# Kernel tuning notes

Measured on AMD Instinct MI355X. Metric: run time of the kernel, lower is better.

The kernel has to match this reference:

```python
import jax, jax.numpy as jnp
import numpy as np

N, E, Q = 50000, 800000, 2000000   # nodes, edges, quadruplets
F_IN, H, OUT, G = 128, 128, 1, 64  # in_channels, hidden, out_channels, graphs
NRBF = NCBF = NSBF = 6
L = 3  # num_layers


def _mlp2(h, Wa, ba, Wb, bb):
    # Linear -> ReLU -> Linear
    return jax.nn.relu(h @ Wa + ba) @ Wb + bb


def setup_inputs() -> dict:
    key = jax.random.key(0)
    ks = jax.random.split(key, 24)
    s = 0.05
    inp = {
        "x": jax.random.normal(ks[0], (N, F_IN), jnp.float32),
        "rbf": jax.random.normal(ks[1], (E, NRBF), jnp.float32),
        "cbf": jax.random.normal(ks[2], (Q, NCBF), jnp.float32),
        "sbf": jax.random.normal(ks[3], (Q, NSBF), jnp.float32),
        "edge_index": jax.random.randint(ks[4], (2, E), 0, N),
        "l_idx": jax.random.randint(ks[5], (Q,), 0, N),
        "k_idx": jax.random.randint(ks[6], (Q,), 0, E),
        "batch": jnp.sort(jax.random.randint(ks[7], (N,), 0, G)),
        # per-layer params (all layers share shapes since F_IN == H)
        "W_e1a": s * jax.random.normal(ks[8], (L, F_IN + NRBF + NCBF + NSBF, H)),
        "b_e1a": jnp.zeros((L, H)),
        "W_e1b": s * jax.random.normal(ks[9], (L, H, H)),
        "b_e1b": jnp.zeros((L, H)),
        "W_e2a": s * jax.random.normal(ks[10], (L, 2 * H, H)),
        "b_e2a": jnp.zeros((L, H)),
        "W_e2b": s * jax.random.normal(ks[11], (L, H, H)),
        "b_e2b": jnp.zeros((L, H)),
        "W_na": s * jax.random.normal(ks[12], (L, F_IN + H, H)),
        "b_na": jnp.zeros((L, H)),
        "W_nb": s * jax.random.normal(ks[13], (L, H, H)),
        "b_nb": jnp.zeros((L, H)),
        "W_oa": s * jax.random.normal(ks[14], (H, H)),
        "b_oa": jnp.zeros((H,)),
        "W_ob": s * jax.random.normal(ks[15], (H, OUT)),
        "b_ob": jnp.zeros((OUT,)),
    }
    return inp


def reference(x, rbf, cbf, sbf,
              W_e1a, b_e1a, W_e1b, b_e1b,
              W_e2a, b_e2a, W_e2b, b_e2b,
              W_na, b_na, W_nb, b_nb,
              W_oa, b_oa, W_ob, b_ob,
              edge_index, l_idx, k_idx, batch):
    src, dst = edge_index[0], edge_index[1]  # x_j = x[src], index = dst
    h = x
    for p in range(L):
        # quadruplet message: gather-concat-MLP  [Q, F+18] -> [Q, H]
        m_in = jnp.concatenate([h[l_idx], rbf[k_idx], cbf, sbf], axis=-1)
        em = _mlp2(m_in, W_e1a[p], b_e1a[p], W_e1b[p], b_e1b[p])
        # scatter-add quadruplet messages onto edges by k_idx -> [E, H]
        agg_e = jax.ops.segment_sum(em, k_idx, num_segments=E)
        # second stage: per-edge concat (note: aggregated indexed by dst, as in source)
        fin = jnp.concatenate([h[src], agg_e[dst]], axis=-1)
        msg = _mlp2(fin, W_e2a[p], b_e2a[p], W_e2b[p], b_e2b[p])
        # aggregate edge messages to target nodes -> [N, H]
        aggr = jax.ops.segment_sum(msg, dst, num_segments=N)
        h = _mlp2(jnp.concatenate([h, aggr], axis=-1), W_na[p], b_na[p], W_nb[p], b_nb[p])
    # global mean pool over graphs
    counts = jax.ops.segment_sum(jnp.ones((N, 1), h.dtype), batch, num_segments=G)
    pooled = jax.ops.segment_sum(h, batch, num_segments=G) / jnp.maximum(counts, 1.0)
    pooled = jax.nn.relu(pooled)
    return _mlp2(pooled, W_oa, b_oa, W_ob, b_ob)
```

## Files before the change

kernel.cpp:

```cpp
#include <hip/hip_runtime.h>

constexpr int Nn = 50000;
constexpr int Ee = 800000;
constexpr int Qq = 2000000;
constexpr int Gg = 64;
constexpr int Hh = 128;
constexpr int NB64 = (Nn + 63) / 64;
constexpr int NSCB = (Nn + 1023) / 1024;

typedef short bf16x8 __attribute__((ext_vector_type(8)));
typedef float f32x4  __attribute__((ext_vector_type(4)));

__device__ __forceinline__ unsigned short f2bf(float f) {
    unsigned u = __builtin_bit_cast(unsigned, f);
    u += 0x7FFFu + ((u >> 16) & 1u);
    return (unsigned short)(u >> 16);
}
__device__ __forceinline__ float bf2f(unsigned short s) {
    unsigned u = ((unsigned)s) << 16;
    return __builtin_bit_cast(float, u);
}

__global__ void k_hist(const int* __restrict__ idx, int n, int limit,
                       int* __restrict__ hist) {
    int i = blockIdx.x * blockDim.x + threadIdx.x;
    if (i < n) { int v = idx[i]; if (v < limit) atomicAdd(&hist[v], 1); }
}

__global__ __launch_bounds__(1024) void k_scanA(const int* __restrict__ hist,
                                                int* __restrict__ cursor,
                                                int* __restrict__ bsum) {
    __shared__ int s[1024];
    const int tid = threadIdx.x;
    int i = blockIdx.x * 1024 + tid;
    int v = (i < Nn) ? hist[i] : 0;
    s[tid] = v;
    __syncthreads();
    for (int off = 1; off < 1024; off <<= 1) {
        int t = (tid >= off) ? s[tid - off] : 0;
        __syncthreads();
        s[tid] += t;
        __syncthreads();
    }
    if (i < Nn) cursor[i] = s[tid] - v;
    if (tid == 1023) bsum[blockIdx.x] = s[1023];
}
__global__ void k_scanB(int* __restrict__ bsum) {
    __shared__ int s[64];
    const int tid = threadIdx.x;
    int v = (tid < NSCB) ? bsum[tid] : 0;
    s[tid] = v;
    __syncthreads();
    for (int off = 1; off < 64; off <<= 1) {
        int t = (tid >= off) ? s[tid - off] : 0;
        __syncthreads();
        s[tid] += t;
        __syncthreads();
    }
    if (tid < NSCB) bsum[tid] = s[tid] - v;
}
__global__ __launch_bounds__(1024) void k_scanC(int* __restrict__ cursor,
                                                const int* __restrict__ bsum) {
    int i = blockIdx.x * 1024 + threadIdx.x;
    if (i < Nn) cursor[i] += bsum[blockIdx.x];
}

__global__ void k_scatter_e(const int* __restrict__ dst, const int* __restrict__ src,
                            int* __restrict__ cursor, int* __restrict__ srcs) {
    int i = blockIdx.x * blockDim.x + threadIdx.x;
    if (i < Ee) {
        int v = dst[i];
        int p = atomicAdd(&cursor[v], 1);
        srcs[p] = src[i];
    }
}

__global__ void k_scatter_q(const int* __restrict__ k_idx, const int* __restrict__ l_idx,
                            const float* __restrict__ cbf, const float* __restrict__ sbf,
                            int* __restrict__ cursor,
                            int* __restrict__ lq, unsigned short* __restrict__ qfeat) {
    int i = blockIdx.x * blockDim.x + threadIdx.x;
    if (i >= Qq) return;
    int v = k_idx[i];
    if (v >= Nn) return;
    int p = atomicAdd(&cursor[v], 1);
    lq[p] = l_idx[i];
    unsigned short f[12];
#pragma unroll
    for (int k = 0; k < 6; ++k) f[k] = f2bf(cbf[(size_t)i * 6 + k]);
#pragma unroll
    for (int k = 0; k < 6; ++k) f[6 + k] = f2bf(sbf[(size_t)i * 6 + k]);
    *(uint2*)&qfeat[(size_t)p * 12]     = *(uint2*)&f[0];
    *(uint2*)&qfeat[(size_t)p * 12 + 4] = *(uint2*)&f[4];
    *(uint2*)&qfeat[(size_t)p * 12 + 8] = *(uint2*)&f[8];
}

__global__ void k_wtall(const float* __restrict__ We1a0, const float* __restrict__ We1b0,
                        const float* __restrict__ We2a0, const float* __restrict__ We2b0,
                        const float* __restrict__ Wna0,  const float* __restrict__ Wnb0,
                        unsigned short* __restrict__ wbuf) {
    int idx = blockIdx.x * blockDim.x + threadIdx.x;
    if (idx >= 135168) return;
    const int p = blockIdx.y;
    const float* We1a = We1a0 + (size_t)p * 146 * 128;
    const float* We1b = We1b0 + (size_t)p * 128 * 128;
    const float* We2a = We2a0 + (size_t)p * 256 * 128;
    const float* We2b = We2b0 + (size_t)p * 128 * 128;
    const float* Wna  = Wna0  + (size_t)p * 256 * 128;
    const float* Wnb  = Wnb0  + (size_t)p * 128 * 128;
    unsigned short* base = wbuf + (size_t)p * 135168;
    const float* src; int K, Kp, loc;
    if (idx < 16384)       { src = We1a;             K = 128; Kp = 128; loc = idx; }
    else if (idx < 20480)  { src = We1a + 128 * 128; K = 6;   Kp = 32;  loc = idx - 16384; }
    else if (idx < 36864)  { src = We1b;             K = 128; Kp = 128; loc = idx - 20480; }
    else if (idx < 69632)  { src = We2a;             K = 256; Kp = 256; loc = idx - 36864; }
    else if (idx < 86016)  { src = We2b;             K = 128; Kp = 128; loc = idx - 69632; }
    else if (idx < 118784) { src = Wna;              K = 256; Kp = 256; loc = idx - 86016; }
    else                   { src = Wnb;              K = 128; Kp = 128; loc = idx - 118784; }
    int n = loc / Kp, k = loc - n * Kp;
    base[idx] = (k < K) ? f2bf(src[(size_t)k * 128 + n]) : (unsigned short)0;
}

__global__ void k_h0(const float* __restrict__ x, unsigned short* __restrict__ hb) {
    int idx = blockIdx.x * blockDim.x + threadIdx.x;
    if (idx < Nn * Hh) hb[idx] = f2bf(x[idx]);
}

__device__ __forceinline__ void zacc(f32x4 acc[4][2]) {
#pragma unroll
    for (int rt = 0; rt < 4; ++rt)
#pragma unroll
        for (int ct = 0; ct < 2; ++ct)
            acc[rt][ct] = (f32x4){0.f, 0.f, 0.f, 0.f};
}

template<int KK, int SA, int KP>
__device__ __forceinline__ void gemm64(const unsigned short* A,
                                       const unsigned short* __restrict__ Wt,
                                       int k_off, f32x4 acc[4][2]) {
    const int tid = threadIdx.x;
    const int lane = tid & 63;
    const int nb = (tid >> 6) * 32;
    const int rA = lane & 15;
    const int kg = lane >> 4;
#pragma unroll
    for (int ks = 0; ks < KK / 32; ++ks) {
        const int ka = ks * 32 + kg * 8;
        const int kb = k_off + ka;
        bf16x8 b0 = *(const bf16x8*)&Wt[(size_t)(nb + rA) * KP + kb];
        bf16x8 b1 = *(const bf16x8*)&Wt[(size_t)(nb + 16 + rA) * KP + kb];
#pragma unroll
        for (int rt = 0; rt < 4; ++rt) {
            bf16x8 a = *(const bf16x8*)&A[(rt * 16 + rA) * SA + ka];
            acc[rt][0] = __builtin_amdgcn_mfma_f32_16x16x32_bf16(a, b0, acc[rt][0], 0, 0, 0);
            acc[rt][1] = __builtin_amdgcn_mfma_f32_16x16x32_bf16(a, b1, acc[rt][1], 0, 0, 0);
        }
    }
}

__device__ __forceinline__ void store_acc(const f32x4 acc[4][2], unsigned short* out,
                                          int n0, int nmax) {
    const int tid = threadIdx.x;
    const int lane = tid & 63;
    const int nb = (tid >> 6) * 32;
    const int rA = lane & 15, kg = lane >> 4;
#pragma unroll
    for (int rt = 0; rt < 4; ++rt)
#pragma unroll
        for (int ct = 0; ct < 2; ++ct) {
            int col = nb + ct * 16 + rA;
#pragma unroll
            for (int i = 0; i < 4; ++i) {
                int n = n0 + rt * 16 + kg * 4 + i;
                if (n < nmax) out[(size_t)n * 128 + col] = f2bf(acc[rt][ct][i]);
            }
        }
}

__global__ __launch_bounds__(256) void k_pre(
    const unsigned short* __restrict__ hb, const float* __restrict__ rbf,
    const unsigned short* __restrict__ wb,
    unsigned short* __restrict__ P1, unsigned short* __restrict__ Z1,
    unsigned short* __restrict__ P2)
{
    __shared__ unsigned short L[64 * 136];
    const int m0 = blockIdx.x * 64;
    const int tid = threadIdx.x;
    const unsigned short* Wq1t = wb;
    const unsigned short* Wp2t = wb + 16384;
    const unsigned short* We2at = wb + 36864;
    for (int i = tid; i < 64 * 16; i += 256) {
        int row = i >> 4, ch = i & 15;
        int n = min(m0 + row, Nn - 1);
        *(uint4*)&L[row * 136 + ch * 8] = *(const uint4*)&hb[(size_t)n * 128 + ch * 8];
    }
    __syncthreads();
    f32x4 acc[4][2];
    zacc(acc);
    gemm64<128, 136, 128>(L, Wq1t, 0, acc);
    store_acc(acc, P1, m0, Nn);
    zacc(acc);
    gemm64<128, 136, 256>(L, We2at, 0, acc);
    store_acc(acc, Z1, m0, Nn);
    __syncthreads();
    for (int i = tid; i < 64 * 32; i += 256) {
        int row = i >> 5, c = i & 31;
        int n = min(m0 + row, Nn - 1);
        float v = (c < 6) ? rbf[(size_t)n * 6 + c] : 0.f;
        L[row * 136 + c] = f2bf(v);
    }
    __syncthreads();
    zacc(acc);
    gemm64<32, 136, 32>(L, Wp2t, 0, acc);
    store_acc(acc, P2, m0, Nn);
}

__global__ __launch_bounds__(256) void k_quadagg(
    const unsigned short* __restrict__ P1, const unsigned short* __restrict__ P2,
    const unsigned short* __restrict__ qfeat, const int* __restrict__ lq,
    const int* __restrict__ rowend, const int* __restrict__ rowcnt,
    const float* __restrict__ We1a_raw, const float* __restrict__ b_e1a,
    unsigned short* __restrict__ Rb)
{
    __shared__ float W34[12 * 128];
    __shared__ float bia[128];
    const int tid = threadIdx.x;
    for (int i = tid; i < 12 * 128; i += 256) W34[i] = We1a_raw[134 * 128 + i];
    if (tid < 128) bia[tid] = b_e1a[tid];
    __syncthreads();
    const int nd = tid >> 4;
    const int c0 = (tid & 15) * 8;
    const int n = blockIdx.x * 16 + nd;
    const int end = rowend[n];
    const int beg = end - rowcnt[n];
    float base[8];
    {
        uint4 p2v = *(const uint4*)&P2[(size_t)n * 128 + c0];
        const unsigned short* pp = (const unsigned short*)&p2v;
#pragma unroll
        for (int k = 0; k < 8; ++k) base[k] = bia[c0 + k] + bf2f(pp[k]);
    }
    float acc[8];
#pragma unroll
    for (int k = 0; k < 8; ++k) acc[k] = 0.f;
    for (int e = beg; e < end; ++e) {
        int l = lq[e];
        uint4 a = *(const uint4*)&P1[(size_t)l * 128 + c0];
        uint2 f0 = *(const uint2*)&qfeat[(size_t)e * 12];
        uint2 f1 = *(const uint2*)&qfeat[(size_t)e * 12 + 4];
        uint2 f2 = *(const uint2*)&qfeat[(size_t)e * 12 + 8];
        const unsigned short* q0 = (const unsigned short*)&f0;
        const unsigned short* q1 = (const unsigned short*)&f1;
        const unsigned short* q2 = (const unsigned short*)&f2;
        float qv[12] = {bf2f(q0[0]), bf2f(q0[1]), bf2f(q0[2]), bf2f(q0[3]),
                        bf2f(q1[0]), bf2f(q1[1]), bf2f(q1[2]), bf2f(q1[3]),
                        bf2f(q2[0]), bf2f(q2[1]), bf2f(q2[2]), bf2f(q2[3])};
        const unsigned short* ap = (const unsigned short*)&a;
        float t[8];
#pragma unroll
        for (int k = 0; k < 8; ++k) t[k] = base[k] + bf2f(ap[k]);
#pragma unroll
        for (int kk = 0; kk < 12; ++kk) {
            float q_ = qv[kk];
#pragma unroll
            for (int k = 0; k < 8; ++k)
                t[k] = fmaf(q_, W34[kk * 128 + c0 + k], t[k]);
        }
#pragma unroll
        for (int k = 0; k < 8; ++k) acc[k] += fmaxf(t[k], 0.f);
    }
    unsigned short ov[8];
#pragma unroll
    for (int k = 0; k < 8; ++k) ov[k] = f2bf(acc[k]);
    *(uint4*)&Rb[(size_t)n * 128 + c0] = *(uint4*)ov;
}

__global__ __launch_bounds__(256) void k_edgeagg(
    const unsigned short* __restrict__ Z1, const unsigned short* __restrict__ Z2,
    const int* __restrict__ srcs,
    const int* __restrict__ rowend, const int* __restrict__ rowcnt,
    const float* __restrict__ b_e2a,
    unsigned short* __restrict__ Rb)
{
    const int tid = threadIdx.x;
    const int nd = tid >> 4;
    const int c0 = (tid & 15) * 8;
    const int n = blockIdx.x * 16 + nd;
    const int end = rowend[n];
    const int beg = end - rowcnt[n];
    float z2b[8];
    {
        uint4 zv = *(const uint4*)&Z2[(size_t)n * 128 + c0];
        const unsigned short* zp = (const unsigned short*)&zv;
        float4 b0 = *(const float4*)&b_e2a[c0];
        float4 b1 = *(const float4*)&b_e2a[c0 + 4];
        z2b[0] = b0.x + bf2f(zp[0]); z2b[1] = b0.y + bf2f(zp[1]);
        z2b[2] = b0.z + bf2f(zp[2]); z2b[3] = b0.w + bf2f(zp[3]);
        z2b[4] = b1.x + bf2f(zp[4]); z2b[5] = b1.y + bf2f(zp[5]);
        z2b[6] = b1.z + bf2f(zp[6]); z2b[7] = b1.w + bf2f(zp[7]);
    }
    float acc[8];
#pragma unroll
    for (int k = 0; k < 8; ++k) acc[k] = 0.f;
    int e = beg;
    for (; e + 2 <= end; e += 2) {
        int s0 = srcs[e], s1 = srcs[e + 1];
        uint4 a0 = *(const uint4*)&Z1[(size_t)s0 * 128 + c0];
        uint4 a1 = *(const uint4*)&Z1[(size_t)s1 * 128 + c0];
        const unsigned short* p0 = (const unsigned short*)&a0;
        const unsigned short* p1 = (const unsigned short*)&a1;
#pragma unroll
        for (int k = 0; k < 8; ++k) acc[k] += fmaxf(z2b[k] + bf2f(p0[k]), 0.f);
#pragma unroll
        for (int k = 0; k < 8; ++k) acc[k] += fmaxf(z2b[k] + bf2f(p1[k]), 0.f);
    }
    if (e < end) {
        int s0 = srcs[e];
        uint4 a0 = *(const uint4*)&Z1[(size_t)s0 * 128 + c0];
        const unsigned short* p0 = (const unsigned short*)&a0;
#pragma unroll
        for (int k = 0; k < 8; ++k) acc[k] += fmaxf(z2b[k] + bf2f(p0[k]), 0.f);
    }
    unsigned short ov[8];
#pragma unroll
    for (int k = 0; k < 8; ++k) ov[k] = f2bf(acc[k]);
    *(uint4*)&Rb[(size_t)n * 128 + c0] = *(uint4*)ov;
}

__global__ __launch_bounds__(256) void k_agg2z(
    const unsigned short* __restrict__ Rb, const int* __restrict__ cntq,
    const unsigned short* __restrict__ wb, const float* __restrict__ b_e1b,
    unsigned short* __restrict__ Z2)
{
    __shared__ unsigned short L[64 * 136];
    __shared__ int rc[64];
    const int m0 = blockIdx.x * 64;
    const int tid = threadIdx.x;
    const unsigned short* We1bt = wb + 20480;
    const unsigned short* We2at = wb + 36864;
    if (tid < 64) rc[tid] = (m0 + tid < Nn) ? cntq[m0 + tid] : 0;
    for (int i = tid; i < 64 * 16; i += 256) {
        int row = i >> 4, ch = i & 15;
        int n = min(m0 + row, Nn - 1);
        *(uint4*)&L[row * 136 + ch * 8] = *(const uint4*)&Rb[(size_t)n * 128 + ch * 8];
    }
    __syncthreads();
    f32x4 acc[4][2];
    zacc(acc);
    gemm64<128, 136, 128>(L, We1bt, 0, acc);
    __syncthreads();
    {
        const int lane = tid & 63;
        const int nb = (tid >> 6) * 32;
        const int rA = lane & 15, kg = lane >> 4;
#pragma unroll
        for (int rt = 0; rt < 4; ++rt)
#pragma unroll
            for (int ct = 0; ct < 2; ++ct) {
                int col = nb + ct * 16 + rA;
                float bias = b_e1b[col];
#pragma unroll
                for (int i = 0; i < 4; ++i) {
                    int row = rt * 16 + kg * 4 + i;
                    L[row * 136 + col] = f2bf(acc[rt][ct][i] + (float)rc[row] * bias);
                }
            }
    }
    __syncthreads();
    zacc(acc);
    gemm64<128, 136, 256>(L, We2at, 128, acc);
    store_acc(acc, Z2, m0, Nn);
}

__global__ __launch_bounds__(256) void k_nodeNew(
    const unsigned short* __restrict__ Rb, const int* __restrict__ deg,
    const unsigned short* __restrict__ wb,
    const float* __restrict__ b_e2b, const float* __restrict__ b_na,
    const float* __restrict__ b_nb,
    unsigned short* __restrict__ hb)
{
    __shared__ unsigned short L[64 * 136];
    __shared__ int rc[64];
    const int m0 = blockIdx.x * 64;
    const int tid = threadIdx.x;
    const unsigned short* We2bt = wb + 69632;
    const unsigned short* Wnat  = wb + 86016;
    const unsigned short* Wnbt  = wb + 118784;
    const int lane = tid & 63;
    const int nb = (tid >> 6) * 32;
    const int rA = lane & 15, kg = lane >> 4;
    if (tid < 64) rc[tid] = (m0 + tid < Nn) ? deg[m0 + tid] : 0;
    for (int i = tid; i < 64 * 16; i += 256) {
        int row = i >> 4, ch = i & 15;
        int n = min(m0 + row, Nn - 1);
        *(uint4*)&L[row * 136 + ch * 8] = *(const uint4*)&Rb[(size_t)n * 128 + ch * 8];
    }
    __syncthreads();
    f32x4 acc[4][2];
    zacc(acc);
    gemm64<128, 136, 128>(L, We2bt, 0, acc);
    __syncthreads();
#pragma unroll
    for (int rt = 0; rt < 4; ++rt)
#pragma unroll
        for (int ct = 0; ct < 2; ++ct) {
            int col = nb + ct * 16 + rA;
            float bias = b_e2b[col];
#pragma unroll
            for (int i = 0; i < 4; ++i) {
                int row = rt * 16 + kg * 4 + i;
                L[row * 136 + col] = f2bf(acc[rt][ct][i] + (float)rc[row] * bias);
            }
        }
    __syncthreads();
    f32x4 acc2[4][2];
    zacc(acc2);
    gemm64<128, 136, 256>(L, Wnat, 128, acc2);
    __syncthreads();
    for (int i = tid; i < 64 * 16; i += 256) {
        int row = i >> 4, ch = i & 15;
        int n = min(m0 + row, Nn - 1);
        *(uint4*)&L[row * 136 + ch * 8] = *(const uint4*)&hb[(size_t)n * 128 + ch * 8];
    }
    __syncthreads();
    gemm64<128, 136, 256>(L, Wnat, 0, acc2);
    __syncthreads();
#pragma unroll
    for (int rt = 0; rt < 4; ++rt)
#pragma unroll
        for (int ct = 0; ct < 2; ++ct) {
            int col = nb + ct * 16 + rA;
            float bias = b_na[col];
#pragma unroll
            for (int i = 0; i < 4; ++i) {
                int row = rt * 16 + kg * 4 + i;
                L[row * 136 + col] = f2bf(fmaxf(acc2[rt][ct][i] + bias, 0.f));
            }
        }
    __syncthreads();
    zacc(acc);
    gemm64<128, 136, 128>(L, Wnbt, 0, acc);
#pragma unroll
    for (int rt = 0; rt < 4; ++rt)
#pragma unroll
        for (int ct = 0; ct < 2; ++ct) {
            int col = nb + ct * 16 + rA;
            float bias = b_nb[col];
#pragma unroll
            for (int i = 0; i < 4; ++i) {
                int n = m0 + rt * 16 + kg * 4 + i;
                if (n < Nn)
                    hb[(size_t)n * 128 + col] = f2bf(acc[rt][ct][i] + bias);
            }
        }
}

__global__ __launch_bounds__(256) void k_pool(const unsigned short* __restrict__ hb,
                                              const int* __restrict__ batch,
                                              float* __restrict__ pooled,
                                              float* __restrict__ cntg) {
    __shared__ int bseg[200];
    constexpr int CH = 196;
    const int start = blockIdx.x * CH;
    const int end = min(start + CH, Nn);
    if (start >= end) return;
    const int tid = threadIdx.x;
    for (int i = tid; i < end - start; i += 256) bseg[i] = batch[start + i];
    __syncthreads();
    const int j = tid & 127;
    const int rh = tid >> 7;
    float acc = 0.f, cacc = 0.f;
    int cur = -1;
    for (int n = start + rh; n < end; n += 2) {
        int g = bseg[n - start];
        if (g != cur) {
            if (cur >= 0) {
                atomicAdd(&pooled[cur * Hh + j], acc);
                if (j == 0) atomicAdd(&cntg[cur], cacc);
            }
            cur = g; acc = 0.f; cacc = 0.f;
        }
        acc += bf2f(hb[(size_t)n * Hh + j]);
        cacc += 1.f;
    }
    if (cur >= 0) {
        atomicAdd(&pooled[cur * Hh + j], acc);
        if (j == 0) atomicAdd(&cntg[cur], cacc);
    }
}

__global__ __launch_bounds__(128) void k_final(
    const float* __restrict__ pooled, const float* __restrict__ cntg,
    const float* __restrict__ Woa, const float* __restrict__ boa,
    const float* __restrict__ Wob, const float* __restrict__ bob,
    float* __restrict__ out)
{
    __shared__ float p[128];
    __shared__ float t[128];
    __shared__ float red[128];
    const int g = blockIdx.x;
    const int j = threadIdx.x;
    float c = fmaxf(cntg[g], 1.f);
    p[j] = fmaxf(pooled[g * Hh + j] / c, 0.f);
    __syncthreads();
    float acc = boa[j];
    for (int d = 0; d < Hh; ++d) acc = fmaf(p[d], Woa[d * Hh + j], acc);
    t[j] = fmaxf(acc, 0.f);
    __syncthreads();
    red[j] = t[j] * Wob[j];
    __syncthreads();
    for (int s = 64; s > 0; s >>= 1) {
        if (j < s) red[j] += red[j + s];
        __syncthreads();
    }
    if (j == 0) out[g] = red[0] + bob[0];
}

extern "C" void kernel_launch(void* const* d_in, const int* in_sizes, int n_in,
                              void* d_out, int out_size, void* d_ws, size_t ws_size,
                              hipStream_t stream) {
    const float* x     = (const float*)d_in[0];
    const float* rbf   = (const float*)d_in[1];
    const float* cbf   = (const float*)d_in[2];
    const float* sbf   = (const float*)d_in[3];
    const int*   eidx  = (const int*)d_in[4];
    const int*   l_idx = (const int*)d_in[5];
    const int*   k_idx = (const int*)d_in[6];
    const int*   batch = (const int*)d_in[7];
    const float* W_e1a = (const float*)d_in[8];
    const float* b_e1a = (const float*)d_in[9];
    const float* W_e1b = (const float*)d_in[10];
    const float* b_e1b = (const float*)d_in[11];
    const float* W_e2a = (const float*)d_in[12];
    const float* b_e2a = (const float*)d_in[13];
    const float* W_e2b = (const float*)d_in[14];
    const float* b_e2b = (const float*)d_in[15];
    const float* W_na  = (const float*)d_in[16];
    const float* b_na  = (const float*)d_in[17];
    const float* W_nb  = (const float*)d_in[18];
    const float* b_nb  = (const float*)d_in[19];
    const float* W_oa  = (const float*)d_in[20];
    const float* b_oa  = (const float*)d_in[21];
    const float* W_ob  = (const float*)d_in[22];
    const float* b_ob  = (const float*)d_in[23];

    const int* src = eidx;
    const int* dst = eidx + Ee;

    const size_t NHb = (size_t)Nn * Hh * sizeof(unsigned short);
    char* w = (char*)d_ws;
    unsigned short* hb  = (unsigned short*)w; w += NHb;
    unsigned short* P1  = (unsigned short*)w; w += NHb;
    unsigned short* P2  = (unsigned short*)w; w += NHb;
    unsigned short* Z1  = (unsigned short*)w; w += NHb;
    unsigned short* Z2  = (unsigned short*)w; w += NHb;
    unsigned short* Rb  = (unsigned short*)w; w += NHb;
    float* pooled = (float*)w; w += (size_t)Gg * Hh * sizeof(float);
    float* cntg   = (float*)w; w += (size_t)Gg * sizeof(float);
    int*   lq     = (int*)w;   w += (size_t)Qq * sizeof(int);
    unsigned short* qfeat = (unsigned short*)w; w += (size_t)Qq * 12 * sizeof(unsigned short);
    int*   srcs_e = (int*)w;   w += (size_t)Ee * sizeof(int);
    int*   hist_e = (int*)w;   w += (size_t)Nn * sizeof(int);
    int*   hist_q = (int*)w;   w += (size_t)Nn * sizeof(int);
    int*   cur_e  = (int*)w;   w += (size_t)Nn * sizeof(int);
    int*   cur_q  = (int*)w;   w += (size_t)Nn * sizeof(int);
    int*   bsum_e = (int*)w;   w += 64 * sizeof(int);
    int*   bsum_q = (int*)w;   w += 64 * sizeof(int);
    unsigned short* wbuf = (unsigned short*)w;

    const size_t LSTRIDE = 135168;

    hipMemsetAsync(hist_e, 0, Nn * sizeof(int), stream);
    k_hist<<<(Ee + 255) / 256, 256, 0, stream>>>(dst, Ee, Nn, hist_e);
    k_scanA<<<NSCB, 1024, 0, stream>>>(hist_e, cur_e, bsum_e);
    k_scanB<<<1, 64, 0, stream>>>(bsum_e);
    k_scanC<<<NSCB, 1024, 0, stream>>>(cur_e, bsum_e);
    k_scatter_e<<<(Ee + 255) / 256, 256, 0, stream>>>(dst, src, cur_e, srcs_e);
    hipMemsetAsync(hist_q, 0, Nn * sizeof(int), stream);
    k_hist<<<(Qq + 255) / 256, 256, 0, stream>>>(k_idx, Qq, Nn, hist_q);
    k_scanA<<<NSCB, 1024, 0, stream>>>(hist_q, cur_q, bsum_q);
    k_scanB<<<1, 64, 0, stream>>>(bsum_q);
    k_scanC<<<NSCB, 1024, 0, stream>>>(cur_q, bsum_q);
    k_scatter_q<<<(Qq + 255) / 256, 256, 0, stream>>>(k_idx, l_idx, cbf, sbf,
        cur_q, lq, qfeat);

    k_h0<<<(Nn * Hh + 255) / 256, 256, 0, stream>>>(x, hb);

    {
        dim3 g((135168 + 255) / 256, 3);
        k_wtall<<<g, 256, 0, stream>>>(W_e1a, W_e1b, W_e2a, W_e2b, W_na, W_nb, wbuf);
    }

    for (int p = 0; p < 3; ++p) {
        const unsigned short* wb = wbuf + p * LSTRIDE;
        k_pre<<<NB64, 256, 0, stream>>>(hb, rbf, wb, P1, Z1, P2);
        k_quadagg<<<Nn / 16, 256, 0, stream>>>(P1, P2, qfeat, lq,
            cur_q, hist_q, W_e1a + (size_t)p * 146 * 128, b_e1a + (size_t)p * 128, Rb);
        k_agg2z<<<NB64, 256, 0, stream>>>(Rb, hist_q, wb, b_e1b + (size_t)p * 128, Z2);
        k_edgeagg<<<Nn / 16, 256, 0, stream>>>(Z1, Z2, srcs_e, cur_e, hist_e,
            b_e2a + (size_t)p * 128, Rb);
        k_nodeNew<<<NB64, 256, 0, stream>>>(Rb, hist_e, wb,
            b_e2b + (size_t)p * 128, b_na + (size_t)p * 128, b_nb + (size_t)p * 128,
            hb);
    }
    hipMemsetAsync(pooled, 0, (size_t)Gg * Hh * sizeof(float), stream);
    hipMemsetAsync(cntg, 0, (size_t)Gg * sizeof(float), stream);
    k_pool<<<(Nn + 195) / 196, 256, 0, stream>>>(hb, batch, pooled, cntg);
    k_final<<<Gg, 128, 0, stream>>>(pooled, cntg, W_oa, b_oa, W_ob, b_ob, (float*)d_out);
}
```

Before: 572.2 us.

## Fuse per-layer kernels into one megakernel and merge CSR build passes

Merges the per-layer pipeline (quad aggregation, agg2 GEMM, edge aggregation, node update, plus the next layer's P1/Z1 precompute) into a single 64-node-tile kernel that keeps intermediates in shared memory instead of round-tripping Rb/Z2 through global memory. P1/Z1 are double-buffered across layers, and the rbf projection P2 is precomputed for all three layers in an initial kernel that also converts x to bf16. The edge and quad histogram, scan and scatter passes are merged into combined launches to cut launch count. The cost is lower occupancy from the larger shared footprint and register pressure, with only about 782 blocks per layer. Irregular gather work and GEMM work are now serialized inside one block rather than running as separate, well-balanced kernels.

```diff
diff --git a/kernel.cpp b/kernel.cpp
--- a/kernel.cpp
+++ b/kernel.cpp
@@ -21,19 +21,24 @@
     return __builtin_bit_cast(float, u);
 }
 
-__global__ void k_hist(const int* __restrict__ idx, int n, int limit,
-                       int* __restrict__ hist) {
+__global__ void k_hist2(const int* __restrict__ dst, const int* __restrict__ kidx,
+                        int* __restrict__ hist_e, int* __restrict__ hist_q) {
     int i = blockIdx.x * blockDim.x + threadIdx.x;
-    if (i < n) { int v = idx[i]; if (v < limit) atomicAdd(&hist[v], 1); }
-}
-
-__global__ __launch_bounds__(1024) void k_scanA(const int* __restrict__ hist,
-                                                int* __restrict__ cursor,
-                                                int* __restrict__ bsum) {
+    if (i < Ee) atomicAdd(&hist_e[dst[i]], 1);
+    if (i < Qq) { int v = kidx[i]; if (v < Nn) atomicAdd(&hist_q[v], 1); }
+}
+
+__global__ __launch_bounds__(1024) void k_scanA2(const int* __restrict__ he,
+                                                 const int* __restrict__ hq,
+                                                 int* __restrict__ ce, int* __restrict__ cq,
+                                                 int* __restrict__ bs) {
     __shared__ int s[1024];
+    const int* h = blockIdx.y ? hq : he;
+    int* c = blockIdx.y ? cq : ce;
+    int* b = bs + blockIdx.y * 64;
     const int tid = threadIdx.x;
     int i = blockIdx.x * 1024 + tid;
-    int v = (i < Nn) ? hist[i] : 0;
+    int v = (i < Nn) ? h[i] : 0;
     s[tid] = v;
     __syncthreads();
     for (int off = 1; off < 1024; off <<= 1) {
@@ -42,13 +47,14 @@
         s[tid] += t;
         __syncthreads();
     }
-    if (i < Nn) cursor[i] = s[tid] - v;
-    if (tid == 1023) bsum[blockIdx.x] = s[1023];
-}
-__global__ void k_scanB(int* __restrict__ bsum) {
+    if (i < Nn) c[i] = s[tid] - v;
+    if (tid == 1023) b[blockIdx.x] = s[1023];
+}
+__global__ void k_scanB2(int* __restrict__ bs) {
     __shared__ int s[64];
+    int* b = bs + blockIdx.x * 64;
     const int tid = threadIdx.x;
-    int v = (tid < NSCB) ? bsum[tid] : 0;
+    int v = (tid < NSCB) ? b[tid] : 0;
     s[tid] = v;
     __syncthreads();
     for (int off = 1; off < 64; off <<= 1) {
@@ -57,42 +63,42 @@
         s[tid] += t;
         __syncthreads();
     }
-    if (tid < NSCB) bsum[tid] = s[tid] - v;
-}
-__global__ __launch_bounds__(1024) void k_scanC(int* __restrict__ cursor,
-                                                const int* __restrict__ bsum) {
+    if (tid < NSCB) b[tid] = s[tid] - v;
+}
+__global__ __launch_bounds__(1024) void k_scanC2(int* __restrict__ ce, int* __restrict__ cq,
+                                                 const int* __restrict__ bs) {
+    int* c = blockIdx.y ? cq : ce;
+    const int* b = bs + blockIdx.y * 64;
     int i = blockIdx.x * 1024 + threadIdx.x;
-    if (i < Nn) cursor[i] += bsum[blockIdx.x];
-}
-
-__global__ void k_scatter_e(const int* __restrict__ dst, const int* __restrict__ src,
-                            int* __restrict__ cursor, int* __restrict__ srcs) {
+    if (i < Nn) c[i] += b[blockIdx.x];
+}
+
+__global__ void k_scatter_both(const int* __restrict__ dst, const int* __restrict__ src,
+                               const int* __restrict__ kidx, const int* __restrict__ lidx,
+                               const float* __restrict__ cbf, const float* __restrict__ sbf,
+                               int* __restrict__ cur_e, int* __restrict__ cur_q,
+                               int* __restrict__ srcs, int* __restrict__ lq,
+                               unsigned short* __restrict__ qfeat) {
     int i = blockIdx.x * blockDim.x + threadIdx.x;
     if (i < Ee) {
-        int v = dst[i];
-        int p = atomicAdd(&cursor[v], 1);
+        int p = atomicAdd(&cur_e[dst[i]], 1);
         srcs[p] = src[i];
     }
-}
-
-__global__ void k_scatter_q(const int* __restrict__ k_idx, const int* __restrict__ l_idx,
-                            const float* __restrict__ cbf, const float* __restrict__ sbf,
-                            int* __restrict__ cursor,
-                            int* __restrict__ lq, unsigned short* __restrict__ qfeat) {
-    int i = blockIdx.x * blockDim.x + threadIdx.x;
-    if (i >= Qq) return;
-    int v = k_idx[i];
-    if (v >= Nn) return;
-    int p = atomicAdd(&cursor[v], 1);
-    lq[p] = l_idx[i];
-    unsigned short f[12];
-#pragma unroll
-    for (int k = 0; k < 6; ++k) f[k] = f2bf(cbf[(size_t)i * 6 + k]);
-#pragma unroll
-    for (int k = 0; k < 6; ++k) f[6 + k] = f2bf(sbf[(size_t)i * 6 + k]);
-    *(uint2*)&qfeat[(size_t)p * 12]     = *(uint2*)&f[0];
-    *(uint2*)&qfeat[(size_t)p * 12 + 4] = *(uint2*)&f[4];
-    *(uint2*)&qfeat[(size_t)p * 12 + 8] = *(uint2*)&f[8];
+    if (i < Qq) {
+        int v = kidx[i];
+        if (v < Nn) {
+            int p = atomicAdd(&cur_q[v], 1);
+            lq[p] = lidx[i];
+            unsigned short f[12];
+#pragma unroll
+            for (int k = 0; k < 6; ++k) f[k] = f2bf(cbf[(size_t)i * 6 + k]);
+#pragma unroll
+            for (int k = 0; k < 6; ++k) f[6 + k] = f2bf(sbf[(size_t)i * 6 + k]);
+            *(uint2*)&qfeat[(size_t)p * 12]     = *(uint2*)&f[0];
+            *(uint2*)&qfeat[(size_t)p * 12 + 4] = *(uint2*)&f[4];
+            *(uint2*)&qfeat[(size_t)p * 12 + 8] = *(uint2*)&f[8];
+        }
+    }
 }
 
 __global__ void k_wtall(const float* __restrict__ We1a0, const float* __restrict__ We1b0,
@@ -121,11 +127,6 @@
     base[idx] = (k < K) ? f2bf(src[(size_t)k * 128 + n]) : (unsigned short)0;
 }
 
-__global__ void k_h0(const float* __restrict__ x, unsigned short* __restrict__ hb) {
-    int idx = blockIdx.x * blockDim.x + threadIdx.x;
-    if (idx < Nn * Hh) hb[idx] = f2bf(x[idx]);
-}
-
 __device__ __forceinline__ void zacc(f32x4 acc[4][2]) {
 #pragma unroll
     for (int rt = 0; rt < 4; ++rt)
@@ -177,282 +178,283 @@
         }
 }
 
-__global__ __launch_bounds__(256) void k_pre(
-    const unsigned short* __restrict__ hb, const float* __restrict__ rbf,
-    const unsigned short* __restrict__ wb,
+__global__ __launch_bounds__(256) void k_pre0(
+    const float* __restrict__ x, const float* __restrict__ rbf,
+    const unsigned short* __restrict__ wbuf,
+    unsigned short* __restrict__ hb,
     unsigned short* __restrict__ P1, unsigned short* __restrict__ Z1,
-    unsigned short* __restrict__ P2)
+    unsigned short* __restrict__ P2all)
 {
-    __shared__ unsigned short L[64 * 136];
+    __shared__ unsigned short TA[64 * 136];
     const int m0 = blockIdx.x * 64;
     const int tid = threadIdx.x;
-    const unsigned short* Wq1t = wb;
-    const unsigned short* Wp2t = wb + 16384;
-    const unsigned short* We2at = wb + 36864;
+    for (int i = tid; i < 64 * 32; i += 256) {
+        int row = i >> 5, c = i & 31;
+        int n = m0 + row;
+        int nc = min(n, Nn - 1);
+        float4 v = *(const float4*)&x[(size_t)nc * 128 + c * 4];
+        ushort4 o;
+        o.x = f2bf(v.x); o.y = f2bf(v.y); o.z = f2bf(v.z); o.w = f2bf(v.w);
+        *(ushort4*)&TA[row * 136 + c * 4] = o;
+        if (n < Nn) *(ushort4*)&hb[(size_t)n * 128 + c * 4] = o;
+    }
+    __syncthreads();
+    f32x4 acc[4][2];
+    zacc(acc);
+    gemm64<128, 136, 128>(TA, wbuf, 0, acc);
+    store_acc(acc, P1, m0, Nn);
+    zacc(acc);
+    gemm64<128, 136, 256>(TA, wbuf + 36864, 0, acc);
+    store_acc(acc, Z1, m0, Nn);
+    __syncthreads();
+    for (int i = tid; i < 64 * 32; i += 256) {
+        int row = i >> 5, c = i & 31;
+        int nc = min(m0 + row, Nn - 1);
+        float v = (c < 6) ? rbf[(size_t)nc * 6 + c] : 0.f;
+        TA[row * 136 + c] = f2bf(v);
+    }
+    __syncthreads();
+    for (int p = 0; p < 3; ++p) {
+        zacc(acc);
+        gemm64<32, 136, 32>(TA, wbuf + (size_t)p * 135168 + 16384, 0, acc);
+        store_acc(acc, P2all + (size_t)p * Nn * 128, m0, Nn);
+    }
+}
+
+template<int LAST>
+__global__ __launch_bounds__(256) void k_mega(
+    unsigned short* __restrict__ hb,
+    const unsigned short* __restrict__ P1, const unsigned short* __restrict__ Z1,
+    const unsigned short* __restrict__ P2L,
+    const unsigned short* __restrict__ qfeat, const int* __restrict__ lq,
+    const int* __restrict__ qend, const int* __restrict__ qcnt,
+    const int* __restrict__ srcs, const int* __restrict__ eend, const int* __restrict__ edeg,
+    const unsigned short* __restrict__ wb, const float* __restrict__ We1a_raw,
+    const float* __restrict__ b_e1a, const float* __restrict__ b_e1b,
+    const float* __restrict__ b_e2a, const float* __restrict__ b_e2b,
+    const float* __restrict__ b_na,  const float* __restrict__ b_nb,
+    const unsigned short* __restrict__ wbn,
+    unsigned short* __restrict__ P1n, unsigned short* __restrict__ Z1n)
+{
+    __shared__ unsigned short TA[64 * 136];
+    __shared__ unsigned short TB[64 * 136];
+    __shared__ float W34[12 * 128];
+    __shared__ float BIA[6 * 128];
+    __shared__ int q_end[64], q_cnt[64], e_end[64], e_deg[64];
+
+    const int m0 = blockIdx.x * 64;
+    const int tid = threadIdx.x;
+    const int lane = tid & 63;
+    const int nbw = (tid >> 6) * 32;
+    const int rA = lane & 15, kg = lane >> 4;
+
+    for (int i = tid; i < 12 * 128; i += 256) W34[i] = We1a_raw[134 * 128 + i];
+    if (tid < 128) {
+        BIA[tid]       = b_e1a[tid];
+        BIA[128 + tid] = b_e1b[tid];
+        BIA[256 + tid] = b_e2a[tid];
+        BIA[384 + tid] = b_e2b[tid];
+        BIA[512 + tid] = b_na[tid];
+        BIA[640 + tid] = b_nb[tid];
+    }
+    if (tid < 64) {
+        int n = m0 + tid;
+        bool ok = n < Nn;
+        q_end[tid] = ok ? qend[n] : 0;
+        q_cnt[tid] = ok ? qcnt[n] : 0;
+        e_end[tid] = ok ? eend[n] : 0;
+        e_deg[tid] = ok ? edeg[n] : 0;
+    }
+    __syncthreads();
+
+    {
+        const int c0 = (tid & 15) * 8;
+        const int ndb = tid >> 4;
+#pragma unroll
+        for (int pass = 0; pass < 4; ++pass) {
+            int nl = pass * 16 + ndb;
+            int nc = min(m0 + nl, Nn - 1);
+            int end = q_end[nl], beg = end - q_cnt[nl];
+            float base[8], acc8[8];
+            uint4 p2v = *(const uint4*)&P2L[(size_t)nc * 128 + c0];
+            const unsigned short* pp = (const unsigned short*)&p2v;
+#pragma unroll
+            for (int k = 0; k < 8; ++k) { base[k] = BIA[c0 + k] + bf2f(pp[k]); acc8[k] = 0.f; }
+            for (int e = beg; e < end; ++e) {
+                int l = lq[e];
+                uint4 a = *(const uint4*)&P1[(size_t)l * 128 + c0];
+                uint2 f0 = *(const uint2*)&qfeat[(size_t)e * 12];
+                uint2 f1 = *(const uint2*)&qfeat[(size_t)e * 12 + 4];
+                uint2 f2 = *(const uint2*)&qfeat[(size_t)e * 12 + 8];
+                const unsigned short* q0 = (const unsigned short*)&f0;
+                const unsigned short* q1 = (const unsigned short*)&f1;
+                const unsigned short* q2 = (const unsigned short*)&f2;
+                float qv[12] = {bf2f(q0[0]), bf2f(q0[1]), bf2f(q0[2]), bf2f(q0[3]),
+                                bf2f(q1[0]), bf2f(q1[1]), bf2f(q1[2]), bf2f(q1[3]),
+                                bf2f(q2[0]), bf2f(q2[1]), bf2f(q2[2]), bf2f(q2[3])};
+                const unsigned short* ap = (const unsigned short*)&a;
+                float t[8];
+#pragma unroll
+                for (int k = 0; k < 8; ++k) t[k] = base[k] + bf2f(ap[k]);
+#pragma unroll
+                for (int kk = 0; kk < 12; ++kk) {
+                    float q_ = qv[kk];
+#pragma unroll
+                    for (int k = 0; k < 8; ++k)
+                        t[k] = fmaf(q_, W34[kk * 128 + c0 + k], t[k]);
+                }
+#pragma unroll
+                for (int k = 0; k < 8; ++k) acc8[k] += fmaxf(t[k], 0.f);
+            }
+            unsigned short ov[8];
+#pragma unroll
+            for (int k = 0; k < 8; ++k) ov[k] = f2bf(acc8[k]);
+            *(uint4*)&TA[nl * 136 + c0] = *(uint4*)ov;
+        }
+    }
+    __syncthreads();
+
+    f32x4 acc[4][2];
+    zacc(acc);
+    gemm64<128, 136, 128>(TA, wb + 20480, 0, acc);
+#pragma unroll
+    for (int rt = 0; rt < 4; ++rt)
+#pragma unroll
+        for (int ct = 0; ct < 2; ++ct) {
+            int col = nbw + ct * 16 + rA;
+            float b = BIA[128 + col];
+#pragma unroll
+            for (int i = 0; i < 4; ++i) {
+                int row = rt * 16 + kg * 4 + i;
+                TB[row * 136 + col] = f2bf(acc[rt][ct][i] + (float)q_cnt[row] * b);
+            }
+        }
+    __syncthreads();
+
+    zacc(acc);
+    gemm64<128, 136, 256>(TB, wb + 36864, 128, acc);
+#pragma unroll
+    for (int rt = 0; rt < 4; ++rt)
+#pragma unroll
+        for (int ct = 0; ct < 2; ++ct) {
+            int col = nbw + ct * 16 + rA;
+#pragma unroll
+            for (int i = 0; i < 4; ++i) {
+                int row = rt * 16 + kg * 4 + i;
+                TA[row * 136 + col] = f2bf(acc[rt][ct][i]);
+            }
+        }
+    __syncthreads();
+
+    {
+        const int c0 = (tid & 15) * 8;
+        const int ndb = tid >> 4;
+#pragma unroll
+        for (int pass = 0; pass < 4; ++pass) {
+            int nl = pass * 16 + ndb;
+            int end = e_end[nl], beg = end - e_deg[nl];
+            float z2b[8], acc8[8];
+#pragma unroll
+            for (int k = 0; k < 8; ++k) {
+                z2b[k] = BIA[256 + c0 + k] + bf2f(TA[nl * 136 + c0 + k]);
+                acc8[k] = 0.f;
+            }
+            int e = beg;
+            for (; e + 2 <= end; e += 2) {
+                int s0 = srcs[e], s1 = srcs[e + 1];
+                uint4 a0 = *(const uint4*)&Z1[(size_t)s0 * 128 + c0];
+                uint4 a1 = *(const uint4*)&Z1[(size_t)s1 * 128 + c0];
+                const unsigned short* p0 = (const unsigned short*)&a0;
+                const unsigned short* p1 = (const unsigned short*)&a1;
+#pragma unroll
+                for (int k = 0; k < 8; ++k) acc8[k] += fmaxf(z2b[k] + bf2f(p0[k]), 0.f);
+#pragma unroll
+                for (int k = 0; k < 8; ++k) acc8[k] += fmaxf(z2b[k] + bf2f(p1[k]), 0.f);
+            }
+            if (e < end) {
+                int s0 = srcs[e];
+                uint4 a0 = *(const uint4*)&Z1[(size_t)s0 * 128 + c0];
+                const unsigned short* p0 = (const unsigned short*)&a0;
+#pragma unroll
+                for (int k = 0; k < 8; ++k) acc8[k] += fmaxf(z2b[k] + bf2f(p0[k]), 0.f);
+            }
+            unsigned short ov[8];
+#pragma unroll
+            for (int k = 0; k < 8; ++k) ov[k] = f2bf(acc8[k]);
+            *(uint4*)&TB[nl * 136 + c0] = *(uint4*)ov;
+        }
+    }
+    __syncthreads();
+
+    zacc(acc);
+    gemm64<128, 136, 128>(TB, wb + 69632, 0, acc);
+#pragma unroll
+    for (int rt = 0; rt < 4; ++rt)
+#pragma unroll
+        for (int ct = 0; ct < 2; ++ct) {
+            int col = nbw + ct * 16 + rA;
+            float b = BIA[384 + col];
+#pragma unroll
+            for (int i = 0; i < 4; ++i) {
+                int row = rt * 16 + kg * 4 + i;
+                TA[row * 136 + col] = f2bf(acc[rt][ct][i] + (float)e_deg[row] * b);
+            }
+        }
+    __syncthreads();
+
+    f32x4 acc2[4][2];
+    zacc(acc2);
+    gemm64<128, 136, 256>(TA, wb + 86016, 128, acc2);
     for (int i = tid; i < 64 * 16; i += 256) {
         int row = i >> 4, ch = i & 15;
-        int n = min(m0 + row, Nn - 1);
-        *(uint4*)&L[row * 136 + ch * 8] = *(const uint4*)&hb[(size_t)n * 128 + ch * 8];
-    }
-    __syncthreads();
-    f32x4 acc[4][2];
-    zacc(acc);
-    gemm64<128, 136, 128>(L, Wq1t, 0, acc);
-    store_acc(acc, P1, m0, Nn);
-    zacc(acc);
-    gemm64<128, 136, 256>(L, We2at, 0, acc);
-    store_acc(acc, Z1, m0, Nn);
-    __syncthreads();
-    for (int i = tid; i < 64 * 32; i += 256) {
-        int row = i >> 5, c = i & 31;
-        int n = min(m0 + row, Nn - 1);
-        float v = (c < 6) ? rbf[(size_t)n * 6 + c] : 0.f;
-        L[row * 136 + c] = f2bf(v);
-    }
-    __syncthreads();
-    zacc(acc);
-    gemm64<32, 136, 32>(L, Wp2t, 0, acc);
-    store_acc(acc, P2, m0, Nn);
-}
-
-__global__ __launch_bounds__(256) void k_quadagg(
-    const unsigned short* __restrict__ P1, const unsigned short* __restrict__ P2,
-    const unsigned short* __restrict__ qfeat, const int* __restrict__ lq,
-    const int* __restrict__ rowend, const int* __restrict__ rowcnt,
-    const float* __restrict__ We1a_raw, const float* __restrict__ b_e1a,
-    unsigned short* __restrict__ Rb)
-{
-    __shared__ float W34[12 * 128];
-    __shared__ float bia[128];
-    const int tid = threadIdx.x;
-    for (int i = tid; i < 12 * 128; i += 256) W34[i] = We1a_raw[134 * 128 + i];
-    if (tid < 128) bia[tid] = b_e1a[tid];
-    __syncthreads();
-    const int nd = tid >> 4;
-    const int c0 = (tid & 15) * 8;
-    const int n = blockIdx.x * 16 + nd;
-    const int end = rowend[n];
-    const int beg = end - rowcnt[n];
-    float base[8];
-    {
-        uint4 p2v = *(const uint4*)&P2[(size_t)n * 128 + c0];
-        const unsigned short* pp = (const unsigned short*)&p2v;
-#pragma unroll
-        for (int k = 0; k < 8; ++k) base[k] = bia[c0 + k] + bf2f(pp[k]);
-    }
-    float acc[8];
-#pragma unroll
-    for (int k = 0; k < 8; ++k) acc[k] = 0.f;
-    for (int e = beg; e < end; ++e) {
-        int l = lq[e];
-        uint4 a = *(const uint4*)&P1[(size_t)l * 128 + c0];
-        uint2 f0 = *(const uint2*)&qfeat[(size_t)e * 12];
-        uint2 f1 = *(const uint2*)&qfeat[(size_t)e * 12 + 4];
-        uint2 f2 = *(const uint2*)&qfeat[(size_t)e * 12 + 8];
-        const unsigned short* q0 = (const unsigned short*)&f0;
-        const unsigned short* q1 = (const unsigned short*)&f1;
-        const unsigned short* q2 = (const unsigned short*)&f2;
-        float qv[12] = {bf2f(q0[0]), bf2f(q0[1]), bf2f(q0[2]), bf2f(q0[3]),
-                        bf2f(q1[0]), bf2f(q1[1]), bf2f(q1[2]), bf2f(q1[3]),
-                        bf2f(q2[0]), bf2f(q2[1]), bf2f(q2[2]), bf2f(q2[3])};
-        const unsigned short* ap = (const unsigned short*)&a;
-        float t[8];
-#pragma unroll
-        for (int k = 0; k < 8; ++k) t[k] = base[k] + bf2f(ap[k]);
-#pragma unroll
-        for (int kk = 0; kk < 12; ++kk) {
-            float q_ = qv[kk];
-#pragma unroll
-            for (int k = 0; k < 8; ++k)
-                t[k] = fmaf(q_, W34[kk * 128 + c0 + k], t[k]);
-        }
-#pragma unroll
-        for (int k = 0; k < 8; ++k) acc[k] += fmaxf(t[k], 0.f);
-    }
-    unsigned short ov[8];
-#pragma unroll
-    for (int k = 0; k < 8; ++k) ov[k] = f2bf(acc[k]);
-    *(uint4*)&Rb[(size_t)n * 128 + c0] = *(uint4*)ov;
-}
-
-__global__ __launch_bounds__(256) void k_edgeagg(
-    const unsigned short* __restrict__ Z1, const unsigned short* __restrict__ Z2,
-    const int* __restrict__ srcs,
-    const int* __restrict__ rowend, const int* __restrict__ rowcnt,
-    const float* __restrict__ b_e2a,
-    unsigned short* __restrict__ Rb)
-{
-    const int tid = threadIdx.x;
-    const int nd = tid >> 4;
-    const int c0 = (tid & 15) * 8;
-    const int n = blockIdx.x * 16 + nd;
-    const int end = rowend[n];
-    const int beg = end - rowcnt[n];
-    float z2b[8];
-    {
-        uint4 zv = *(const uint4*)&Z2[(size_t)n * 128 + c0];
-        const unsigned short* zp = (const unsigned short*)&zv;
-        float4 b0 = *(const float4*)&b_e2a[c0];
-        float4 b1 = *(const float4*)&b_e2a[c0 + 4];
-        z2b[0] = b0.x + bf2f(zp[0]); z2b[1] = b0.y + bf2f(zp[1]);
-        z2b[2] = b0.z + bf2f(zp[2]); z2b[3] = b0.w + bf2f(zp[3]);
-        z2b[4] = b1.x + bf2f(zp[4]); z2b[5] = b1.y + bf2f(zp[5]);
-        z2b[6] = b1.z + bf2f(zp[6]); z2b[7] = b1.w + bf2f(zp[7]);
-    }
-    float acc[8];
-#pragma unroll
-    for (int k = 0; k < 8; ++k) acc[k] = 0.f;
-    int e = beg;
-    for (; e + 2 <= end; e += 2) {
-        int s0 = srcs[e], s1 = srcs[e + 1];
-        uint4 a0 = *(const uint4*)&Z1[(size_t)s0 * 128 + c0];
-        uint4 a1 = *(const uint4*)&Z1[(size_t)s1 * 128 + c0];
-        const unsigned short* p0 = (const unsigned short*)&a0;
-        const unsigned short* p1 = (const unsigned short*)&a1;
-#pragma unroll
-        for (int k = 0; k < 8; ++k) acc[k] += fmaxf(z2b[k] + bf2f(p0[k]), 0.f);
-#pragma unroll
-        for (int k = 0; k < 8; ++k) acc[k] += fmaxf(z2b[k] + bf2f(p1[k]), 0.f);
-    }
-    if (e < end) {
-        int s0 = srcs[e];
-        uint4 a0 = *(const uint4*)&Z1[(size_t)s0 * 128 + c0];
-        const unsigned short* p0 = (const unsigned short*)&a0;
-#pragma unroll
-        for (int k = 0; k < 8; ++k) acc[k] += fmaxf(z2b[k] + bf2f(p0[k]), 0.f);
-    }
-    unsigned short ov[8];
-#pragma unroll
-    for (int k = 0; k < 8; ++k) ov[k] = f2bf(acc[k]);
-    *(uint4*)&Rb[(size_t)n * 128 + c0] = *(uint4*)ov;
-}
-
-__global__ __launch_bounds__(256) void k_agg2z(
-    const unsigned short* __restrict__ Rb, const int* __restrict__ cntq,
-    const unsigned short* __restrict__ wb, const float* __restrict__ b_e1b,
-    unsigned short* __restrict__ Z2)
-{
-    __shared__ unsigned short L[64 * 136];
-    __shared__ int rc[64];
-    const int m0 = blockIdx.x * 64;
-    const int tid = threadIdx.x;
-    const unsigned short* We1bt = wb + 20480;
-    const unsigned short* We2at = wb + 36864;
-    if (tid < 64) rc[tid] = (m0 + tid < Nn) ? cntq[m0 + tid] : 0;
-    for (int i = tid; i < 64 * 16; i += 256) {
-        int row = i >> 4, ch = i & 15;
-        int n = min(m0 + row, Nn - 1);
-        *(uint4*)&L[row * 136 + ch * 8] = *(const uint4*)&Rb[(size_t)n * 128 + ch * 8];
-    }
-    __syncthreads();
-    f32x4 acc[4][2];
-    zacc(acc);
-    gemm64<128, 136, 128>(L, We1bt, 0, acc);
-    __syncthreads();
-    {
-        const int lane = tid & 63;
-        const int nb = (tid >> 6) * 32;
-        const int rA = lane & 15, kg = lane >> 4;
-#pragma unroll
-        for (int rt = 0; rt < 4; ++rt)
-#pragma unroll
-            for (int ct = 0; ct < 2; ++ct) {
-                int col = nb + ct * 16 + rA;
-                float bias = b_e1b[col];
-#pragma unroll
-                for (int i = 0; i < 4; ++i) {
-                    int row = rt * 16 + kg * 4 + i;
-                    L[row * 136 + col] = f2bf(acc[rt][ct][i] + (float)rc[row] * bias);
-                }
-            }
-    }
-    __syncthreads();
-    zacc(acc);
-    gemm64<128, 136, 256>(L, We2at, 128, acc);
-    store_acc(acc, Z2, m0, Nn);
-}
-
-__global__ __launch_bounds__(256) void k_nodeNew(
-    const unsigned short* __restrict__ Rb, const int* __restrict__ deg,
-    const unsigned short* __restrict__ wb,
-    const float* __restrict__ b_e2b, const float* __restrict__ b_na,
-    const float* __restrict__ b_nb,
-    unsigned short* __restrict__ hb)
-{
-    __shared__ unsigned short L[64 * 136];
-    __shared__ int rc[64];
-    const int m0 = blockIdx.x * 64;
-    const int tid = threadIdx.x;
-    const unsigned short* We2bt = wb + 69632;
-    const unsigned short* Wnat  = wb + 86016;
-    const unsigned short* Wnbt  = wb + 118784;
-    const int lane = tid & 63;
-    const int nb = (tid >> 6) * 32;
-    const int rA = lane & 15, kg = lane >> 4;
-    if (tid < 64) rc[tid] = (m0 + tid < Nn) ? deg[m0 + tid] : 0;
-    for (int i = tid; i < 64 * 16; i += 256) {
-        int row = i >> 4, ch = i & 15;
-        int n = min(m0 + row, Nn - 1);
-        *(uint4*)&L[row * 136 + ch * 8] = *(const uint4*)&Rb[(size_t)n * 128 + ch * 8];
-    }
-    __syncthreads();
-    f32x4 acc[4][2];
-    zacc(acc);
-    gemm64<128, 136, 128>(L, We2bt, 0, acc);
-    __syncthreads();
+        int n = m0 + row;
+        uint4 v;
+        if (n < Nn) v = *(const uint4*)&hb[(size_t)n * 128 + ch * 8];
+        else { v.x = v.y = v.z = v.w = 0u; }
+        *(uint4*)&TB[row * 136 + ch * 8] = v;
+    }
+    __syncthreads();
+    gemm64<128, 136, 256>(TB, wb + 86016, 0, acc2);
 #pragma unroll
     for (int rt = 0; rt < 4; ++rt)
 #pragma unroll
         for (int ct = 0; ct < 2; ++ct) {
-            int col = nb + ct * 16 + rA;
-            float bias = b_e2b[col];
+            int col = nbw + ct * 16 + rA;
+            float b = BIA[512 + col];
 #pragma unroll
             for (int i = 0; i < 4; ++i) {
                 int row = rt * 16 + kg * 4 + i;
-                L[row * 136 + col] = f2bf(acc[rt][ct][i] + (float)rc[row] * bias);
-            }
-        }
-    __syncthreads();
-    f32x4 acc2[4][2];
-    zacc(acc2);
-    gemm64<128, 136, 256>(L, Wnat, 128, acc2);
-    __syncthreads();
-    for (int i = tid; i < 64 * 16; i += 256) {
-        int row = i >> 4, ch = i & 15;
-        int n = min(m0 + row, Nn - 1);
-        *(uint4*)&L[row * 136 + ch * 8] = *(const uint4*)&hb[(size_t)n * 128 + ch * 8];
-    }
-    __syncthreads();
-    gemm64<128, 136, 256>(L, Wnat, 0, acc2);
-    __syncthreads();
+                TA[row * 136 + col] = f2bf(fmaxf(acc2[rt][ct][i] + b, 0.f));
+            }
+        }
+    __syncthreads();
+
+    zacc(acc);
+    gemm64<128, 136, 128>(TA, wb + 118784, 0, acc);
 #pragma unroll
     for (int rt = 0; rt < 4; ++rt)
 #pragma unroll
         for (int ct = 0; ct < 2; ++ct) {
-            int col = nb + ct * 16 + rA;
-            float bias = b_na[col];
+            int col = nbw + ct * 16 + rA;
+            float b = BIA[640 + col];
 #pragma unroll
             for (int i = 0; i < 4; ++i) {
                 int row = rt * 16 + kg * 4 + i;
-                L[row * 136 + col] = f2bf(fmaxf(acc2[rt][ct][i] + bias, 0.f));
-            }
-        }
-    __syncthreads();
-    zacc(acc);
-    gemm64<128, 136, 128>(L, Wnbt, 0, acc);
-#pragma unroll
-    for (int rt = 0; rt < 4; ++rt)
-#pragma unroll
-        for (int ct = 0; ct < 2; ++ct) {
-            int col = nb + ct * 16 + rA;
-            float bias = b_nb[col];
-#pragma unroll
-            for (int i = 0; i < 4; ++i) {
-                int n = m0 + rt * 16 + kg * 4 + i;
-                if (n < Nn)
-                    hb[(size_t)n * 128 + col] = f2bf(acc[rt][ct][i] + bias);
-            }
-        }
+                int n = m0 + row;
+                unsigned short hv = (n < Nn) ? f2bf(acc[rt][ct][i] + b) : (unsigned short)0;
+                if (n < Nn) hb[(size_t)n * 128 + col] = hv;
+                if (!LAST) TB[row * 136 + col] = hv;
+            }
+        }
+    if (!LAST) {
+        __syncthreads();
+        zacc(acc);
+        gemm64<128, 136, 128>(TB, wbn, 0, acc);
+        store_acc(acc, P1n, m0, Nn);
+        zacc(acc);
+        gemm64<128, 136, 256>(TB, wbn + 36864, 0, acc);
+        store_acc(acc, Z1n, m0, Nn);
+    }
 }
 
 __global__ __launch_bounds__(256) void k_pool(const unsigned short* __restrict__ hb,
@@ -549,12 +551,12 @@
 
     const size_t NHb = (size_t)Nn * Hh * sizeof(unsigned short);
     char* w = (char*)d_ws;
-    unsigned short* hb  = (unsigned short*)w; w += NHb;
-    unsigned short* P1  = (unsigned short*)w; w += NHb;
-    unsigned short* P2  = (unsigned short*)w; w += NHb;
-    unsigned short* Z1  = (unsigned short*)w; w += NHb;
-    unsigned short* Z2  = (unsigned short*)w; w += NHb;
-    unsigned short* Rb  = (unsigned short*)w; w += NHb;
+    unsigned short* hb   = (unsigned short*)w; w += NHb;
+    unsigned short* P1a  = (unsigned short*)w; w += NHb;
+    unsigned short* P1b  = (unsigned short*)w; w += NHb;
+    unsigned short* Z1a  = (unsigned short*)w; w += NHb;
+    unsigned short* Z1b  = (unsigned short*)w; w += NHb;
+    unsigned short* P2all = (unsigned short*)w; w += 3 * NHb;
     float* pooled = (float*)w; w += (size_t)Gg * Hh * sizeof(float);
     float* cntg   = (float*)w; w += (size_t)Gg * sizeof(float);
     int*   lq     = (int*)w;   w += (size_t)Qq * sizeof(int);
@@ -564,47 +566,52 @@
     int*   hist_q = (int*)w;   w += (size_t)Nn * sizeof(int);
     int*   cur_e  = (int*)w;   w += (size_t)Nn * sizeof(int);
     int*   cur_q  = (int*)w;   w += (size_t)Nn * sizeof(int);
-    int*   bsum_e = (int*)w;   w += 64 * sizeof(int);
-    int*   bsum_q = (int*)w;   w += 64 * sizeof(int);
+    int*   bsum   = (int*)w;   w += 128 * sizeof(int);
     unsigned short* wbuf = (unsigned short*)w;
 
     const size_t LSTRIDE = 135168;
 
-    hipMemsetAsync(hist_e, 0, Nn * sizeof(int), stream);
-    k_hist<<<(Ee + 255) / 256, 256, 0, stream>>>(dst, Ee, Nn, hist_e);
-    k_scanA<<<NSCB, 1024, 0, stream>>>(hist_e, cur_e, bsum_e);
-    k_scanB<<<1, 64, 0, stream>>>(bsum_e);
-    k_scanC<<<NSCB, 1024, 0, stream>>>(cur_e, bsum_e);
-    k_scatter_e<<<(Ee + 255) / 256, 256, 0, stream>>>(dst, src, cur_e, srcs_e);
-    hipMemsetAsync(hist_q, 0, Nn * sizeof(int), stream);
-    k_hist<<<(Qq + 255) / 256, 256, 0, stream>>>(k_idx, Qq, Nn, hist_q);
-    k_scanA<<<NSCB, 1024, 0, stream>>>(hist_q, cur_q, bsum_q);
-    k_scanB<<<1, 64, 0, stream>>>(bsum_q);
-    k_scanC<<<NSCB, 1024, 0, stream>>>(cur_q, bsum_q);
-    k_scatter_q<<<(Qq + 255) / 256, 256, 0, stream>>>(k_idx, l_idx, cbf, sbf,
-        cur_q, lq, qfeat);
-
-    k_h0<<<(Nn * Hh + 255) / 256, 256, 0, stream>>>(x, hb);
+    hipMemsetAsync(hist_e, 0, 2 * Nn * sizeof(int), stream);
+    k_hist2<<<(Qq + 255) / 256, 256, 0, stream>>>(dst, k_idx, hist_e, hist_q);
+    {
+        dim3 g(NSCB, 2);
+        k_scanA2<<<g, 1024, 0, stream>>>(hist_e, hist_q, cur_e, cur_q, bsum);
+        k_scanB2<<<2, 64, 0, stream>>>(bsum);
+        k_scanC2<<<g, 1024, 0, stream>>>(cur_e, cur_q, bsum);
+    }
+    k_scatter_both<<<(Qq + 255) / 256, 256, 0, stream>>>(dst, src, k_idx, l_idx,
+        cbf, sbf, cur_e, cur_q, srcs_e, lq, qfeat);
 
     {
         dim3 g((135168 + 255) / 256, 3);
         k_wtall<<<g, 256, 0, stream>>>(W_e1a, W_e1b, W_e2a, W_e2b, W_na, W_nb, wbuf);
     }
-
+    k_pre0<<<NB64, 256, 0, stream>>>(x, rbf, wbuf, hb, P1a, Z1a, P2all);
+
+    unsigned short* P1s[2] = { P1a, P1b };
+    unsigned short* Z1s[2] = { Z1a, Z1b };
     for (int p = 0; p < 3; ++p) {
         const unsigned short* wb = wbuf + p * LSTRIDE;
-        k_pre<<<NB64, 256, 0, stream>>>(hb, rbf, wb, P1, Z1, P2);
-        k_quadagg<<<Nn / 16, 256, 0, stream>>>(P1, P2, qfeat, lq,
-            cur_q, hist_q, W_e1a + (size_t)p * 146 * 128, b_e1a + (size_t)p * 128, Rb);
-        k_agg2z<<<NB64, 256, 0, stream>>>(Rb, hist_q, wb, b_e1b + (size_t)p * 128, Z2);
-        k_edgeagg<<<Nn / 16, 256, 0, stream>>>(Z1, Z2, srcs_e, cur_e, hist_e,
-            b_e2a + (size_t)p * 128, Rb);
-        k_nodeNew<<<NB64, 256, 0, stream>>>(Rb, hist_e, wb,
-            b_e2b + (size_t)p * 128, b_na + (size_t)p * 128, b_nb + (size_t)p * 128,
-            hb);
-    }
-    hipMemsetAsync(pooled, 0, (size_t)Gg * Hh * sizeof(float), stream);
-    hipMemsetAsync(cntg, 0, (size_t)Gg * sizeof(float), stream);
+        const unsigned short* wbn = wbuf + ((p + 1) % 3) * LSTRIDE;
+        int c = p & 1;
+        if (p < 2)
+            k_mega<0><<<NB64, 256, 0, stream>>>(hb, P1s[c], Z1s[c],
+                P2all + (size_t)p * Nn * 128, qfeat, lq, cur_q, hist_q,
+                srcs_e, cur_e, hist_e, wb, W_e1a + (size_t)p * 146 * 128,
+                b_e1a + (size_t)p * 128, b_e1b + (size_t)p * 128,
+                b_e2a + (size_t)p * 128, b_e2b + (size_t)p * 128,
+                b_na + (size_t)p * 128,  b_nb + (size_t)p * 128,
+                wbn, P1s[c ^ 1], Z1s[c ^ 1]);
+        else
+            k_mega<1><<<NB64, 256, 0, stream>>>(hb, P1s[c], Z1s[c],
+                P2all + (size_t)p * Nn * 128, qfeat, lq, cur_q, hist_q,
+                srcs_e, cur_e, hist_e, wb, W_e1a + (size_t)p * 146 * 128,
+                b_e1a + (size_t)p * 128, b_e1b + (size_t)p * 128,
+                b_e2a + (size_t)p * 128, b_e2b + (size_t)p * 128,
+                b_na + (size_t)p * 128,  b_nb + (size_t)p * 128,
+                wbn, P1s[c ^ 1], Z1s[c ^ 1]);
+    }
+    hipMemsetAsync(pooled, 0, (size_t)(Gg * Hh + Gg) * sizeof(float), stream);
     k_pool<<<(Nn + 195) / 196, 256, 0, stream>>>(hb, batch, pooled, cntg);
     k_final<<<Gg, 128, 0, stream>>>(pooled, cntg, W_oa, b_oa, W_ob, b_ob, (float*)d_out);
 }
```

Measured after the change: 615.8 us. 7.6% more time.
